# Performance work log

Hardware: AMD Instinct MI355X
Metric: run time of the kernel (lower is better)

The kernel has to match this reference:

```python
import jax, jax.numpy as jnp
import numpy as np
from math import sqrt

B, H, S, D = 4, 16, 2048, 64
NEG = -1000000000.0

def setup_inputs() -> dict:
    key = jax.random.key(0)
    kq, kk, kv, km = jax.random.split(key, 4)
    Q = jax.random.normal(kq, (B, H, S, D), dtype=jnp.float32)
    K = jax.random.normal(kk, (B, H, S, D), dtype=jnp.float32)
    V = jax.random.normal(kv, (B, H, S, D), dtype=jnp.float32)
    mask = jax.random.uniform(km, (B, 1, S, S)) < 0.1
    return {"Q": Q, "K": K, "V": V, "mask": mask}

def reference(Q, K, V, mask) -> jnp.ndarray:
    # scores: [B,H,S,S]
    scores = jnp.einsum('bhqd,bhkd->bhqk', Q, K)
    scores = jnp.where(mask, NEG, scores)
    attn = jax.nn.softmax(scores / sqrt(Q.shape[-1]), axis=-1)
    return jnp.einsum('bhqk,bhkd->bhqd', attn, V)
```

## Files before the change

### kernel.cpp

```cpp
#include <hip/hip_runtime.h>


#define SEQ 2048
#define DIM 64
#define NBH 64
#define LOG2E 1.44269504088896340736f
#define SCL (0.125f * LOG2E)
#define NEG_SCALED -1.25e8f

typedef short bf16x8 __attribute__((ext_vector_type(8)));
typedef float f32x4 __attribute__((ext_vector_type(4)));
typedef float f32x16 __attribute__((ext_vector_type(16)));

static __device__ __forceinline__ unsigned short f2bf(float f) {
    unsigned int u = __float_as_uint(f);
    u += 0x7fffu + ((u >> 16) & 1u);
    return (unsigned short)(u >> 16);
}

#define GLD16(gp, lp) __builtin_amdgcn_global_load_lds( \
    (const __attribute__((address_space(1))) unsigned int*)(gp), \
    (__attribute__((address_space(3))) unsigned int*)(lp), 16, 0, 0)

__global__ __launch_bounds__(256)
void prep_all_kernel(const float* __restrict__ K, const float* __restrict__ V,
                     const int* __restrict__ M,
                     unsigned short* __restrict__ Kb, unsigned short* __restrict__ Vt,
                     unsigned int* __restrict__ Mpt) {
    const int x = blockIdx.x;
    const int t = threadIdx.x;
    if (x < 4096) {
        size_t i0 = ((size_t)x * 256 + t) * 8;
        float4 a = *(const float4*)(K + i0);
        float4 b = *(const float4*)(K + i0 + 4);
        union { uint4 u; unsigned short s[8]; } w;
        w.s[0] = f2bf(a.x); w.s[1] = f2bf(a.y); w.s[2] = f2bf(a.z); w.s[3] = f2bf(a.w);
        w.s[4] = f2bf(b.x); w.s[5] = f2bf(b.y); w.s[6] = f2bf(b.z); w.s[7] = f2bf(b.w);
        *(uint4*)(Kb + i0) = w.u;
    } else if (x < 6144) {
        __shared__ __align__(16) unsigned short T[64 * 64];
        const int vb = x - 4096;
        const int bh = vb >> 5;
        const int k0 = (vb & 31) * 64;
        {
            const int kk = t >> 2;
            const int c  = t & 3;
            const int u  = (kk & ~12) | ((kk & 4) << 1) | ((kk & 8) >> 1);
            const int cs = c ^ ((u >> 3) & 3);
            const float* vp = V + ((size_t)bh * SEQ + k0 + kk) * DIM + c * 16;
            union { uint4 q[2]; unsigned short s[16]; } w;
            #pragma unroll
            for (int j = 0; j < 16; ++j) w.s[j] = f2bf(vp[j]);
            *(uint4*)&T[u * 64 + cs * 16]     = w.q[0];
            *(uint4*)&T[u * 64 + cs * 16 + 8] = w.q[1];
        }
        __syncthreads();
        {
            const int kc = t & 7;
            const int dp = t >> 3;
            const int ch = (dp >> 3) ^ (kc & 3);
            const unsigned int* T32 = (const unsigned int*)T;
            union { uint4 u; unsigned short s[8]; } o0, o1;
            #pragma unroll
            for (int i = 0; i < 8; ++i) {
                unsigned int v = T32[(8 * kc + i) * 32 + ch * 8 + (dp & 7)];
                o0.s[i] = (unsigned short)v;
                o1.s[i] = (unsigned short)(v >> 16);
            }
            unsigned short* op = Vt + ((size_t)bh * DIM + 2 * dp) * SEQ + k0 + 8 * kc;
            *(uint4*)op         = o0.u;
            *(uint4*)(op + SEQ) = o1.u;
        }
    } else {
        __shared__ unsigned int Wt[64][8];
        const int m  = x - 6144;
        const int b  = m >> 8;
        const int q0 = ((m >> 3) & 31) * 64;
        const int k0 = (m & 7) * 256;
        const int w  = t >> 6, l = t & 63;
        #pragma unroll 4
        for (int row = 0; row < 16; ++row) {
            const int q = q0 + w * 16 + row;
            int4 v4 = *(const int4*)(M + ((size_t)b * SEQ + q) * SEQ + k0 + l * 4);
            unsigned int nib = (unsigned int)(v4.x != 0) | ((unsigned int)(v4.y != 0) << 1)
                             | ((unsigned int)(v4.z != 0) << 2) | ((unsigned int)(v4.w != 0) << 3);
            unsigned int v = nib << (4 * (l & 7));
            v |= __shfl_xor(v, 1);
            v |= __shfl_xor(v, 2);
            v |= __shfl_xor(v, 4);
            if ((l & 7) == 0) Wt[w * 16 + row][l >> 3] = v;
        }
        __syncthreads();
        {
            const int q = t & 63, g0 = t >> 6;
            #pragma unroll
            for (int gg = 0; gg < 2; ++gg) {
                const int g = g0 + gg * 4;
                Mpt[((size_t)b * 64 + (k0 >> 5) + g) * SEQ + q0 + q] = Wt[q][g];
            }
        }
    }
}

__global__ __launch_bounds__(256, 4)
void attn_main_kernel(const float* __restrict__ Q,
                      const unsigned short* __restrict__ Kb,
                      const unsigned short* __restrict__ Vt,
                      const unsigned int* __restrict__ Mpt,
                      float* __restrict__ O)
{
    const int bh   = blockIdx.y;
    const int b    = bh >> 4;
    const int q0   = blockIdx.x * 128;
    const int tid  = threadIdx.x;
    const int wave = tid >> 6;
    const int lane = tid & 63;
    const int h    = lane >> 5;
    const int q32  = lane & 31;

    __shared__ __align__(16) unsigned short Kt[2][32 * 64];
    __shared__ __align__(16) unsigned short Vs[2][64 * 32];

    const unsigned short* Kbh = Kb + (size_t)bh * SEQ * DIM;
    const unsigned short* Vbh = Vt + (size_t)bh * SEQ * DIM;

    bf16x8 qf[4];
    {
        const float* qp = Q + ((size_t)bh * SEQ + q0 + wave * 32 + q32) * DIM + h * 8;
        #pragma unroll
        for (int dc = 0; dc < 4; ++dc) {
            float4 xx = *(const float4*)(qp + dc * 16);
            float4 yy = *(const float4*)(qp + dc * 16 + 4);
            qf[dc][0] = (short)f2bf(xx.x * SCL); qf[dc][1] = (short)f2bf(xx.y * SCL);
            qf[dc][2] = (short)f2bf(xx.z * SCL); qf[dc][3] = (short)f2bf(xx.w * SCL);
            qf[dc][4] = (short)f2bf(yy.x * SCL); qf[dc][5] = (short)f2bf(yy.y * SCL);
            qf[dc][6] = (short)f2bf(yy.z * SCL); qf[dc][7] = (short)f2bf(yy.w * SCL);
        }
    }

    const int kkey  = wave * 8 + (lane >> 3);
    const int kclog = (lane & 7) ^ (lane >> 3);
    const unsigned short* kg = Kbh + (size_t)kkey * DIM + kclog * 8;
    const int vd    = wave * 16 + (lane >> 2);
    const int vclog = (lane & 3) ^ ((lane >> 3) & 3);
    const unsigned short* vg = Vbh + (size_t)vd * SEQ + vclog * 8;
    unsigned short* kl[2] = { &Kt[0][wave * 512], &Kt[1][wave * 512] };
    unsigned short* vl[2] = { &Vs[0][wave * 512], &Vs[1][wave * 512] };

    const unsigned int* mp = Mpt + (size_t)b * 64 * SEQ + (q0 + wave * 32 + q32);

    f32x16 acc[2];
    #pragma unroll
    for (int i = 0; i < 16; ++i) { acc[0][i] = 0.f; acc[1][i] = 0.f; }
    float lsum = 0.f;

    GLD16(kg, kl[0]);
    GLD16(vg, vl[0]);

    #pragma unroll 2
    for (int it = 0; it < SEQ / 32; ++it) {
        __syncthreads();

        unsigned int mw = mp[it * SEQ];

        if (it + 1 < SEQ / 32) {
            const unsigned short* kgn = kg + (size_t)(it + 1) * 32 * DIM;
            const unsigned short* vgn = vg + (size_t)(it + 1) * 32;
            int nb = (it + 1) & 1;
            GLD16(kgn, kl[nb]);
            GLD16(vgn, vl[nb]);
        }

        const unsigned short* Ktb = Kt[it & 1];
        const unsigned short* Vsb = Vs[it & 1];

        f32x16 sc;
        #pragma unroll
        for (int i = 0; i < 16; ++i) sc[i] = 0.f;
        #pragma unroll
        for (int dc = 0; dc < 4; ++dc) {
            const int pos = (dc * 2 + h) ^ (q32 & 7);
            bf16x8 kf = *(const bf16x8*)(Ktb + q32 * 64 + pos * 8);
            sc = __builtin_amdgcn_mfma_f32_32x32x16_bf16(kf, qf[dc], sc, 0, 0, 0);
        }

        const unsigned int mq = mw >> (4 * h);
        float pv[16];
        #pragma unroll
        for (int r = 0; r < 16; ++r) {
            const int s = (r & 3) + 8 * (r >> 2);
            float e = __builtin_amdgcn_exp2f(sc[r]);
            pv[r] = ((mq >> s) & 1u) ? 0.f : e;
            lsum += pv[r];
        }
        unsigned int pk[8];
        #pragma unroll
        for (int m = 0; m < 8; ++m) {
            unsigned int u0 = __float_as_uint(pv[2 * m])     + 0x8000u;
            unsigned int u1 = __float_as_uint(pv[2 * m + 1]) + 0x8000u;
            pk[m] = __builtin_amdgcn_perm(u1, u0, 0x07060302u);
        }

        #pragma unroll
        for (int kk = 0; kk < 2; ++kk) {
            union { unsigned int u[4]; bf16x8 v; } fr;
            fr.u[0] = pk[4 * kk + 0];
            fr.u[1] = pk[4 * kk + 1];
            fr.u[2] = pk[4 * kk + 2];
            fr.u[3] = pk[4 * kk + 3];
            #pragma unroll
            for (int dh = 0; dh < 2; ++dh) {
                const int d   = dh * 32 + q32;
                const int pos = (kk * 2 + h) ^ ((q32 >> 1) & 3);
                bf16x8 vf = *(const bf16x8*)(Vsb + d * 32 + pos * 8);
                acc[dh] = __builtin_amdgcn_mfma_f32_32x32x16_bf16(vf, fr.v, acc[dh], 0, 0, 0);
            }
        }
    }

    lsum += __shfl_xor(lsum, 32);
    const float inv = 1.f / lsum;
    float* orow = O + ((size_t)bh * SEQ + q0 + wave * 32 + q32) * DIM;
    #pragma unroll
    for (int dh = 0; dh < 2; ++dh) {
        #pragma unroll
        for (int r23 = 0; r23 < 4; ++r23) {
            float4 w;
            w.x = acc[dh][4 * r23 + 0] * inv;
            w.y = acc[dh][4 * r23 + 1] * inv;
            w.z = acc[dh][4 * r23 + 2] * inv;
            w.w = acc[dh][4 * r23 + 3] * inv;
            *(float4*)(orow + dh * 32 + r23 * 8 + h * 4) = w;
        }
    }
}

__global__ __launch_bounds__(256)
void attn_fallback_kernel(const float* __restrict__ Q,
                          const float* __restrict__ K,
                          const float* __restrict__ V,
                          const int* __restrict__ mask,
                          float* __restrict__ O)
{
    const int bh   = blockIdx.y;
    const int b    = bh >> 4;
    const int q0   = blockIdx.x * 64;
    const int tid  = threadIdx.x;
    const int wave = tid >> 6;
    const int lane = tid & 63;
    const int quad = lane >> 4;
    const int l16  = lane & 15;

    __shared__ __align__(16) unsigned short Klds[32][72];
    __shared__ __align__(16) unsigned short VT[64][40];
    __shared__ __align__(16) unsigned short Plds[4][16][40];

    const float* Qb = Q + (size_t)bh * SEQ * DIM;
    const float* Kb = K + (size_t)bh * SEQ * DIM;
    const float* Vb = V + (size_t)bh * SEQ * DIM;
    const int*   Mb = mask + (size_t)b * SEQ * SEQ;

    const int qrow_frag = q0 + wave * 16 + l16;
    bf16x8 qf0, qf1;
    {
        const float* qp = Qb + (size_t)qrow_frag * DIM + quad * 8;
        #pragma unroll
        for (int i = 0; i < 8; ++i) {
            qf0[i] = (short)f2bf(qp[i]);
            qf1[i] = (short)f2bf(qp[32 + i]);
        }
    }

    f32x4 acc[4];
    #pragma unroll
    for (int dg = 0; dg < 4; ++dg) acc[dg] = (f32x4){0.f, 0.f, 0.f, 0.f};
    float mrowv[4] = {-INFINITY, -INFINITY, -INFINITY, -INFINITY};
    float lrow[4] = {0.f, 0.f, 0.f, 0.f};

    const int skey = tid >> 3;
    const int sd0  = (tid & 7) * 8;
    const int vkey = tid & 31;
    const int vd0  = (tid >> 5) * 8;
    const int qrow_m = q0 + wave * 16 + quad * 4;

    for (int kb = 0; kb < SEQ; kb += 32) {
        __syncthreads();
        {
            const float* kp = Kb + (size_t)(kb + skey) * DIM + sd0;
            union { uint4 u4; unsigned short s[8]; } kw;
            #pragma unroll
            for (int i = 0; i < 8; ++i) kw.s[i] = f2bf(kp[i]);
            *(uint4*)&Klds[skey][sd0] = kw.u4;
        }
        {
            const float* vp = Vb + (size_t)(kb + vkey) * DIM + vd0;
            #pragma unroll
            for (int i = 0; i < 8; ++i) VT[vd0 + i][vkey] = f2bf(vp[i]);
        }
        __syncthreads();

        f32x4 scr[2];
        scr[0] = (f32x4){0.f, 0.f, 0.f, 0.f};
        scr[1] = (f32x4){0.f, 0.f, 0.f, 0.f};
        #pragma unroll
        for (int nt = 0; nt < 2; ++nt) {
            bf16x8 kf0 = *(const bf16x8*)&Klds[nt * 16 + l16][quad * 8];
            bf16x8 kf1 = *(const bf16x8*)&Klds[nt * 16 + l16][32 + quad * 8];
            scr[nt] = __builtin_amdgcn_mfma_f32_16x16x32_bf16(qf0, kf0, scr[nt], 0, 0, 0);
            scr[nt] = __builtin_amdgcn_mfma_f32_16x16x32_bf16(qf1, kf1, scr[nt], 0, 0, 0);
        }

        float x[2][4];
        #pragma unroll
        for (int nt = 0; nt < 2; ++nt)
            #pragma unroll
            for (int r = 0; r < 4; ++r) {
                int mv = Mb[(size_t)(qrow_m + r) * SEQ + kb + nt * 16 + l16];
                x[nt][r] = mv ? NEG_SCALED : scr[nt][r] * 0.125f;
            }

        float p[2][4];
        #pragma unroll
        for (int r = 0; r < 4; ++r) {
            float rm = fmaxf(x[0][r], x[1][r]);
            #pragma unroll
            for (int off = 1; off < 16; off <<= 1)
                rm = fmaxf(rm, __shfl_xor(rm, off, 16));
            float mn = fmaxf(mrowv[r], rm);
            float alpha = exp2f((mrowv[r] - mn) * LOG2E);
            mrowv[r] = mn;
            float p0 = exp2f((x[0][r] - mn) * LOG2E);
            float p1 = exp2f((x[1][r] - mn) * LOG2E);
            p[0][r] = p0; p[1][r] = p1;
            float rs = p0 + p1;
            #pragma unroll
            for (int off = 1; off < 16; off <<= 1)
                rs += __shfl_xor(rs, off, 16);
            lrow[r] = lrow[r] * alpha + rs;
            #pragma unroll
            for (int dg = 0; dg < 4; ++dg)
                acc[dg][r] *= alpha;
        }

        #pragma unroll
        for (int nt = 0; nt < 2; ++nt)
            #pragma unroll
            for (int r = 0; r < 4; ++r)
                Plds[wave][quad * 4 + r][nt * 16 + l16] = f2bf(p[nt][r]);

        bf16x8 pf = *(const bf16x8*)&Plds[wave][l16][quad * 8];

        #pragma unroll
        for (int dg = 0; dg < 4; ++dg) {
            bf16x8 vf = *(const bf16x8*)&VT[dg * 16 + l16][quad * 8];
            acc[dg] = __builtin_amdgcn_mfma_f32_16x16x32_bf16(pf, vf, acc[dg], 0, 0, 0);
        }
    }

    float* Ob = O + (size_t)bh * SEQ * DIM;
    #pragma unroll
    for (int r = 0; r < 4; ++r) {
        float inv = 1.f / lrow[r];
        #pragma unroll
        for (int dg = 0; dg < 4; ++dg)
            Ob[(size_t)(qrow_m + r) * DIM + dg * 16 + l16] = acc[dg][r] * inv;
    }
}

extern "C" void kernel_launch(void* const* d_in, const int* in_sizes, int n_in,
                              void* d_out, int out_size, void* d_ws, size_t ws_size,
                              hipStream_t stream) {
    const float* Q = (const float*)d_in[0];
    const float* K = (const float*)d_in[1];
    const float* V = (const float*)d_in[2];
    const int* mask = (const int*)d_in[3];
    float*        O = (float*)d_out;

    const size_t szK = (size_t)NBH * SEQ * DIM * 2;
    const size_t szV = (size_t)NBH * SEQ * DIM * 2;
    const size_t szM = (size_t)4 * SEQ * (SEQ / 32) * 4;
    const size_t need = szK + szV + szM;

    if (ws_size >= need) {
        unsigned short* Kb = (unsigned short*)d_ws;
        unsigned short* Vt = (unsigned short*)((char*)d_ws + szK);
        unsigned int*  Mpt = (unsigned int*)((char*)d_ws + szK + szV);

        prep_all_kernel<<<dim3(7168), 256, 0, stream>>>(K, V, mask, Kb, Vt, Mpt);
        attn_main_kernel<<<dim3(SEQ / 128, NBH), 256, 0, stream>>>(Q, Kb, Vt, Mpt, O);
    } else {
        attn_fallback_kernel<<<dim3(SEQ / 64, NBH), 256, 0, stream>>>(Q, K, V, mask, O);
    }
}
```

Measured before the change: 277.7 us.

## Process 64-key tiles per iteration and interleave prep kernel block roles

The main attention loop now handles 64 keys per iteration as two 32-key halves, with doubled LDS buffers and four async global-to-LDS loads per step. This halves the barrier count and gives more independent MFMA work between syncs. LDS offsets are precomputed once, and bf16 packing now uses the HIP intrinsic conversion with round-to-nearest instead of a manual add-and-perm. The prep kernel interleaves K-convert, V-transpose and mask-pack blocks modulo 7 so different memory streams run concurrently. In exchange it doubles LDS per block, which may reduce occupancy.

```diff
diff --git a/kernel.cpp b/kernel.cpp
--- a/kernel.cpp
+++ b/kernel.cpp
@@ -1,4 +1,5 @@
 #include <hip/hip_runtime.h>
+#include <hip/hip_bf16.h>
 
 
 #define SEQ 2048
@@ -18,6 +19,12 @@
     return (unsigned short)(u >> 16);
 }
 
+static __device__ __forceinline__ unsigned int pkbf(float a, float b) {
+    __hip_bfloat162 t = __float22bfloat162_rn(make_float2(a, b));
+    union { __hip_bfloat162 h; unsigned int u; } c; c.h = t;
+    return c.u;
+}
+
 #define GLD16(gp, lp) __builtin_amdgcn_global_load_lds( \
     (const __attribute__((address_space(1))) unsigned int*)(gp), \
     (__attribute__((address_space(3))) unsigned int*)(lp), 16, 0, 0)
@@ -27,19 +34,22 @@
                      const int* __restrict__ M,
                      unsigned short* __restrict__ Kb, unsigned short* __restrict__ Vt,
                      unsigned int* __restrict__ Mpt) {
-    const int x = blockIdx.x;
-    const int t = threadIdx.x;
-    if (x < 4096) {
-        size_t i0 = ((size_t)x * 256 + t) * 8;
+    const int x  = blockIdx.x;
+    const int r7 = x % 7;
+    const int g  = x / 7;
+    const int t  = threadIdx.x;
+    if (r7 < 4) {
+        const int idx = g * 4 + r7;
+        size_t i0 = ((size_t)idx * 256 + t) * 8;
         float4 a = *(const float4*)(K + i0);
         float4 b = *(const float4*)(K + i0 + 4);
         union { uint4 u; unsigned short s[8]; } w;
         w.s[0] = f2bf(a.x); w.s[1] = f2bf(a.y); w.s[2] = f2bf(a.z); w.s[3] = f2bf(a.w);
         w.s[4] = f2bf(b.x); w.s[5] = f2bf(b.y); w.s[6] = f2bf(b.z); w.s[7] = f2bf(b.w);
         *(uint4*)(Kb + i0) = w.u;
-    } else if (x < 6144) {
+    } else if (r7 < 6) {
         __shared__ __align__(16) unsigned short T[64 * 64];
-        const int vb = x - 4096;
+        const int vb = g * 2 + (r7 - 4);
         const int bh = vb >> 5;
         const int k0 = (vb & 31) * 64;
         {
@@ -73,10 +83,9 @@
         }
     } else {
         __shared__ unsigned int Wt[64][8];
-        const int m  = x - 6144;
-        const int b  = m >> 8;
-        const int q0 = ((m >> 3) & 31) * 64;
-        const int k0 = (m & 7) * 256;
+        const int b  = g >> 8;
+        const int q0 = ((g >> 3) & 31) * 64;
+        const int k0 = (g & 7) * 256;
         const int w  = t >> 6, l = t & 63;
         #pragma unroll 4
         for (int row = 0; row < 16; ++row) {
@@ -95,8 +104,8 @@
             const int q = t & 63, g0 = t >> 6;
             #pragma unroll
             for (int gg = 0; gg < 2; ++gg) {
-                const int g = g0 + gg * 4;
-                Mpt[((size_t)b * 64 + (k0 >> 5) + g) * SEQ + q0 + q] = Wt[q][g];
+                const int gi = g0 + gg * 4;
+                Mpt[((size_t)b * 64 + (k0 >> 5) + gi) * SEQ + q0 + q] = Wt[q][gi];
             }
         }
     }
@@ -118,8 +127,8 @@
     const int h    = lane >> 5;
     const int q32  = lane & 31;
 
-    __shared__ __align__(16) unsigned short Kt[2][32 * 64];
-    __shared__ __align__(16) unsigned short Vs[2][64 * 32];
+    __shared__ __align__(16) unsigned short Kt[2][4096];
+    __shared__ __align__(16) unsigned short Vs[2][4096];
 
     const unsigned short* Kbh = Kb + (size_t)bh * SEQ * DIM;
     const unsigned short* Vbh = Vt + (size_t)bh * SEQ * DIM;
@@ -140,79 +149,123 @@
 
     const int kkey  = wave * 8 + (lane >> 3);
     const int kclog = (lane & 7) ^ (lane >> 3);
-    const unsigned short* kg = Kbh + (size_t)kkey * DIM + kclog * 8;
+    const unsigned short* kp = Kbh + (size_t)kkey * DIM + kclog * 8;
     const int vd    = wave * 16 + (lane >> 2);
     const int vclog = (lane & 3) ^ ((lane >> 3) & 3);
-    const unsigned short* vg = Vbh + (size_t)vd * SEQ + vclog * 8;
-    unsigned short* kl[2] = { &Kt[0][wave * 512], &Kt[1][wave * 512] };
-    unsigned short* vl[2] = { &Vs[0][wave * 512], &Vs[1][wave * 512] };
-
-    const unsigned int* mp = Mpt + (size_t)b * 64 * SEQ + (q0 + wave * 32 + q32);
+    const unsigned short* vp = Vbh + (size_t)vd * SEQ + vclog * 8;
+
+    int kofs[4], vofs[4];
+    #pragma unroll
+    for (int dc = 0; dc < 4; ++dc)
+        kofs[dc] = q32 * 64 + (((dc * 2 + h) ^ (q32 & 7)) * 8);
+    #pragma unroll
+    for (int kk = 0; kk < 2; ++kk)
+        #pragma unroll
+        for (int dh = 0; dh < 2; ++dh)
+            vofs[kk * 2 + dh] = (dh * 32 + q32) * 32 + (((kk * 2 + h) ^ ((q32 >> 1) & 3)) * 8);
+
+    const unsigned int* mpc = Mpt + (size_t)b * 64 * SEQ + (q0 + wave * 32 + q32);
 
     f32x16 acc[2];
     #pragma unroll
     for (int i = 0; i < 16; ++i) { acc[0][i] = 0.f; acc[1][i] = 0.f; }
     float lsum = 0.f;
 
-    GLD16(kg, kl[0]);
-    GLD16(vg, vl[0]);
-
-    #pragma unroll 2
-    for (int it = 0; it < SEQ / 32; ++it) {
+    {
+        unsigned short* kd = &Kt[0][wave * 512];
+        unsigned short* vdst = &Vs[0][wave * 512];
+        GLD16(kp, kd);
+        GLD16(kp + 2048, kd + 2048);
+        GLD16(vp, vdst);
+        GLD16(vp + 32, vdst + 2048);
+    }
+
+    for (int it = 0; it < SEQ / 64; ++it) {
         __syncthreads();
 
-        unsigned int mw = mp[it * SEQ];
-
-        if (it + 1 < SEQ / 32) {
-            const unsigned short* kgn = kg + (size_t)(it + 1) * 32 * DIM;
-            const unsigned short* vgn = vg + (size_t)(it + 1) * 32;
-            int nb = (it + 1) & 1;
-            GLD16(kgn, kl[nb]);
-            GLD16(vgn, vl[nb]);
+        unsigned int mw0 = mpc[0];
+        unsigned int mw1 = mpc[SEQ];
+        mpc += 2 * SEQ;
+
+        if (it + 1 < SEQ / 64) {
+            const unsigned short* kn = kp + (size_t)(it + 1) * 64 * DIM;
+            const unsigned short* vn = vp + (size_t)(it + 1) * 64;
+            const int nb = (it + 1) & 1;
+            unsigned short* kd = &Kt[nb][wave * 512];
+            unsigned short* vdst = &Vs[nb][wave * 512];
+            GLD16(kn, kd);
+            GLD16(kn + 2048, kd + 2048);
+            GLD16(vn, vdst);
+            GLD16(vn + 32, vdst + 2048);
         }
 
         const unsigned short* Ktb = Kt[it & 1];
         const unsigned short* Vsb = Vs[it & 1];
 
-        f32x16 sc;
-        #pragma unroll
-        for (int i = 0; i < 16; ++i) sc[i] = 0.f;
+        f32x16 sc0, sc1;
+        #pragma unroll
+        for (int i = 0; i < 16; ++i) { sc0[i] = 0.f; sc1[i] = 0.f; }
         #pragma unroll
         for (int dc = 0; dc < 4; ++dc) {
-            const int pos = (dc * 2 + h) ^ (q32 & 7);
-            bf16x8 kf = *(const bf16x8*)(Ktb + q32 * 64 + pos * 8);
-            sc = __builtin_amdgcn_mfma_f32_32x32x16_bf16(kf, qf[dc], sc, 0, 0, 0);
-        }
-
-        const unsigned int mq = mw >> (4 * h);
-        float pv[16];
-        #pragma unroll
-        for (int r = 0; r < 16; ++r) {
-            const int s = (r & 3) + 8 * (r >> 2);
-            float e = __builtin_amdgcn_exp2f(sc[r]);
-            pv[r] = ((mq >> s) & 1u) ? 0.f : e;
-            lsum += pv[r];
-        }
-        unsigned int pk[8];
-        #pragma unroll
-        for (int m = 0; m < 8; ++m) {
-            unsigned int u0 = __float_as_uint(pv[2 * m])     + 0x8000u;
-            unsigned int u1 = __float_as_uint(pv[2 * m + 1]) + 0x8000u;
-            pk[m] = __builtin_amdgcn_perm(u1, u0, 0x07060302u);
+            bf16x8 kf0 = *(const bf16x8*)(Ktb + kofs[dc]);
+            sc0 = __builtin_amdgcn_mfma_f32_32x32x16_bf16(kf0, qf[dc], sc0, 0, 0, 0);
+        }
+        #pragma unroll
+        for (int dc = 0; dc < 4; ++dc) {
+            bf16x8 kf1 = *(const bf16x8*)(Ktb + 2048 + kofs[dc]);
+            sc1 = __builtin_amdgcn_mfma_f32_32x32x16_bf16(kf1, qf[dc], sc1, 0, 0, 0);
+        }
+
+        unsigned int pk0[8];
+        {
+            const unsigned int mq = mw0 >> (4 * h);
+            float pv[16];
+            #pragma unroll
+            for (int r = 0; r < 16; ++r) {
+                const int s = (r & 3) + 8 * (r >> 2);
+                float e = __builtin_amdgcn_exp2f(sc0[r]);
+                pv[r] = ((mq >> s) & 1u) ? 0.f : e;
+                lsum += pv[r];
+            }
+            #pragma unroll
+            for (int m = 0; m < 8; ++m) pk0[m] = pkbf(pv[2 * m], pv[2 * m + 1]);
         }
 
         #pragma unroll
         for (int kk = 0; kk < 2; ++kk) {
             union { unsigned int u[4]; bf16x8 v; } fr;
-            fr.u[0] = pk[4 * kk + 0];
-            fr.u[1] = pk[4 * kk + 1];
-            fr.u[2] = pk[4 * kk + 2];
-            fr.u[3] = pk[4 * kk + 3];
+            fr.u[0] = pk0[4 * kk + 0]; fr.u[1] = pk0[4 * kk + 1];
+            fr.u[2] = pk0[4 * kk + 2]; fr.u[3] = pk0[4 * kk + 3];
             #pragma unroll
             for (int dh = 0; dh < 2; ++dh) {
-                const int d   = dh * 32 + q32;
-                const int pos = (kk * 2 + h) ^ ((q32 >> 1) & 3);
-                bf16x8 vf = *(const bf16x8*)(Vsb + d * 32 + pos * 8);
+                bf16x8 vf = *(const bf16x8*)(Vsb + vofs[kk * 2 + dh]);
+                acc[dh] = __builtin_amdgcn_mfma_f32_32x32x16_bf16(vf, fr.v, acc[dh], 0, 0, 0);
+            }
+        }
+
+        unsigned int pk1[8];
+        {
+            const unsigned int mq = mw1 >> (4 * h);
+            float pv[16];
+            #pragma unroll
+            for (int r = 0; r < 16; ++r) {
+                const int s = (r & 3) + 8 * (r >> 2);
+                float e = __builtin_amdgcn_exp2f(sc1[r]);
+                pv[r] = ((mq >> s) & 1u) ? 0.f : e;
+                lsum += pv[r];
+            }
+            #pragma unroll
+            for (int m = 0; m < 8; ++m) pk1[m] = pkbf(pv[2 * m], pv[2 * m + 1]);
+        }
+
+        #pragma unroll
+        for (int kk = 0; kk < 2; ++kk) {
+            union { unsigned int u[4]; bf16x8 v; } fr;
+            fr.u[0] = pk1[4 * kk + 0]; fr.u[1] = pk1[4 * kk + 1];
+            fr.u[2] = pk1[4 * kk + 2]; fr.u[3] = pk1[4 * kk + 3];
+            #pragma unroll
+            for (int dh = 0; dh < 2; ++dh) {
+                bf16x8 vf = *(const bf16x8*)(Vsb + 2048 + vofs[kk * 2 + dh]);
                 acc[dh] = __builtin_amdgcn_mfma_f32_32x32x16_bf16(vf, fr.v, acc[dh], 0, 0, 0);
             }
         }
@@ -256,7 +309,7 @@
     __shared__ __align__(16) unsigned short Plds[4][16][40];
 
     const float* Qb = Q + (size_t)bh * SEQ * DIM;
-    const float* Kb = K + (size_t)bh * SEQ * DIM;
+    const float* Kbp = K + (size_t)bh * SEQ * DIM;
     const float* Vb = V + (size_t)bh * SEQ * DIM;
     const int*   Mb = mask + (size_t)b * SEQ * SEQ;
 
@@ -286,16 +339,16 @@
     for (int kb = 0; kb < SEQ; kb += 32) {
         __syncthreads();
         {
-            const float* kp = Kb + (size_t)(kb + skey) * DIM + sd0;
+            const float* kpp = Kbp + (size_t)(kb + skey) * DIM + sd0;
             union { uint4 u4; unsigned short s[8]; } kw;
             #pragma unroll
-            for (int i = 0; i < 8; ++i) kw.s[i] = f2bf(kp[i]);
+            for (int i = 0; i < 8; ++i) kw.s[i] = f2bf(kpp[i]);
             *(uint4*)&Klds[skey][sd0] = kw.u4;
         }
         {
-            const float* vp = Vb + (size_t)(kb + vkey) * DIM + vd0;
-            #pragma unroll
-            for (int i = 0; i < 8; ++i) VT[vd0 + i][vkey] = f2bf(vp[i]);
+            const float* vpp = Vb + (size_t)(kb + vkey) * DIM + vd0;
+            #pragma unroll
+            for (int i = 0; i < 8; ++i) VT[vd0 + i][vkey] = f2bf(vpp[i]);
         }
         __syncthreads();
 
@@ -382,12 +435,12 @@
     const size_t need = szK + szV + szM;
 
     if (ws_size >= need) {
-        unsigned short* Kb = (unsigned short*)d_ws;
-        unsigned short* Vt = (unsigned short*)((char*)d_ws + szK);
-        unsigned int*  Mpt = (unsigned int*)((char*)d_ws + szK + szV);
-
-        prep_all_kernel<<<dim3(7168), 256, 0, stream>>>(K, V, mask, Kb, Vt, Mpt);
-        attn_main_kernel<<<dim3(SEQ / 128, NBH), 256, 0, stream>>>(Q, Kb, Vt, Mpt, O);
+        unsigned short* KbW = (unsigned short*)d_ws;
+        unsigned short* VtW = (unsigned short*)((char*)d_ws + szK);
+        unsigned int*  MptW = (unsigned int*)((char*)d_ws + szK + szV);
+
+        prep_all_kernel<<<dim3(7168), 256, 0, stream>>>(K, V, mask, KbW, VtW, MptW);
+        attn_main_kernel<<<dim3(SEQ / 128, NBH), 256, 0, stream>>>(Q, KbW, VtW, MptW, O);
     } else {
         attn_fallback_kernel<<<dim3(SEQ / 64, NBH), 256, 0, stream>>>(Q, K, V, mask, O);
     }
```

Result: slower. 288.7 us (+4.0%).
